# Kernel tuning notes

Hardware: AMD Instinct MI355X
Metric: run time of the kernel (lower is better)

## Reference

```python
import jax, jax.numpy as jnp
import numpy as np

N = 8192
D = 256  # out_feature; input feature dim must equal this per forward math
NEG_BIG = -9e15


def setup_inputs() -> dict:
    key = jax.random.key(0)
    k1, k2, k3 = jax.random.split(key, 3)
    inp = jax.random.normal(k1, (N, D), dtype=jnp.float32)
    adj = jax.random.randint(k2, (N, N), 0, 2, dtype=jnp.int32)
    # attention parameter A: [2*D, 1], xavier-uniform-like scale
    limit = np.sqrt(6.0 / (2 * D + 1)) * np.sqrt(2.0)  # gain('relu') = sqrt(2)
    A = jax.random.uniform(k3, (2 * D, 1), dtype=jnp.float32, minval=-limit, maxval=limit)
    return {"input": inp, "adj": adj, "A": A}


def reference(input, adj, A):
    d = input.shape[-1]
    h1 = input @ A[d:, :]   # [N, 1]
    h2 = input @ A[:d, :]   # [N, 1]
    e = h1 + h2.T           # [N, N] broadcast add
    att = jnp.where(adj > 0, e, jnp.asarray(NEG_BIG, e.dtype))
    att = jax.nn.softmax(att, axis=-1)
    return att @ input      # [N, D]
```

## Files before the change

kernel.cpp:

```cpp
#include <hip/hip_runtime.h>
#include <hip/hip_bf16.h>
#include <stdint.h>

typedef __attribute__((ext_vector_type(8))) short bf16x8;
typedef __attribute__((ext_vector_type(4))) float f32x4;

#define NN 8192
#define DF 256
#define BM 32
#define BK 64
#define KSPLIT 2
#define KCH (NN / KSPLIT)
#define NT (KCH / BK)

static __device__ __forceinline__ unsigned short f2bf(float f) {
  union { float f; unsigned u; } v; v.f = f;
  unsigned r = (v.u + 0x7FFFu + ((v.u >> 16) & 1u)) >> 16;
  return (unsigned short)r;
}

static __device__ __forceinline__ void gl_lds16(const void* g, void* l) {
  __builtin_amdgcn_global_load_lds(
      (const __attribute__((address_space(1))) void*)g,
      (__attribute__((address_space(3))) void*)l, 16, 0, 0);
}

__global__ void k_h2(const float* __restrict__ input, const float* __restrict__ A,
                     float* __restrict__ h2) {
  int gw = (blockIdx.x * blockDim.x + threadIdx.x) >> 6;
  int lane = threadIdx.x & 63;
  float4 x = *reinterpret_cast<const float4*>(&input[(size_t)gw * DF + lane * 4]);
  float4 a = *reinterpret_cast<const float4*>(&A[lane * 4]);
  float p = x.x * a.x + x.y * a.y + x.z * a.z + x.w * a.w;
#pragma unroll
  for (int off = 32; off > 0; off >>= 1) p += __shfl_down(p, off, 64);
  if (lane == 0) h2[gw] = p;
}

__global__ void k_max(const float* __restrict__ h2, float* __restrict__ Mout) {
  __shared__ float sm[4];
  float m = -3.0e38f;
  for (int i = threadIdx.x; i < NN; i += 256) m = fmaxf(m, h2[i]);
#pragma unroll
  for (int off = 32; off > 0; off >>= 1) m = fmaxf(m, __shfl_down(m, off, 64));
  int lane = threadIdx.x & 63, wid = threadIdx.x >> 6;
  if (lane == 0) sm[wid] = m;
  __syncthreads();
  if (threadIdx.x == 0)
    Mout[0] = fmaxf(fmaxf(sm[0], sm[1]), fmaxf(sm[2], sm[3]));
}

__global__ void k_s(const float* __restrict__ h2, const float* __restrict__ Mp,
                    float* __restrict__ sF, unsigned short* __restrict__ sT) {
  int j = blockIdx.x * 256 + threadIdx.x;
  float s = expf(h2[j] - Mp[0]);
  sF[j] = s;
  sT[j] = f2bf(s);
}

__global__ void k_xst(const float* __restrict__ input, const float* __restrict__ sF,
                      unsigned short* __restrict__ XsT) {
  int b = blockIdx.x;
  int jb = b >> 2, cb = b & 3;
  int t = threadIdx.x;
  int j0 = jb * 64 + (t & 15) * 4;
  int c0 = cb * 64 + (t >> 4) * 4;
  float4 x[4]; float s[4];
#pragma unroll
  for (int ii = 0; ii < 4; ii++) {
    x[ii] = *reinterpret_cast<const float4*>(&input[(size_t)(j0 + ii) * DF + c0]);
    s[ii] = sF[j0 + ii];
  }
#pragma unroll
  for (int q = 0; q < 4; q++) {
    ushort4 o;
    o.x = f2bf(reinterpret_cast<const float*>(&x[0])[q] * s[0]);
    o.y = f2bf(reinterpret_cast<const float*>(&x[1])[q] * s[1]);
    o.z = f2bf(reinterpret_cast<const float*>(&x[2])[q] * s[2]);
    o.w = f2bf(reinterpret_cast<const float*>(&x[3])[q] * s[3]);
    *reinterpret_cast<ushort4*>(&XsT[(size_t)(c0 + q) * NN + j0]) = o;
  }
}

__global__ __launch_bounds__(512, 2) void k_gemm(
    const int* __restrict__ adj, const unsigned short* __restrict__ XsT,
    const unsigned short* __restrict__ sT, float* __restrict__ C0,
    float* __restrict__ C1, float* __restrict__ denomPart) {
  __shared__ __align__(16) char Al[3][BM * BK * 4];

  const int tid = threadIdx.x;
  const int lane = tid & 63;
  const int wid = tid >> 6;
  const int wrow = wid >> 2;
  const int wcol = wid & 3;
  const int l15 = lane & 15;
  const int l4 = lane >> 4;

  const int bx = blockIdx.x;
  const int swz = (bx & 7) * 64 + (bx >> 3);
  const int kidx = swz >> 8;
  const int rb = swz & 255;
  const int kbeg = kidx * KCH;
  float* __restrict__ Cout = kidx ? C1 : C0;

  const int srow = tid >> 4;
  const int skb = ((tid & 15) * 16) ^ ((srow & 7) << 4);
  const int* sA = adj + (int64_t)(rb * BM + srow) * NN + kbeg + (skb >> 2);
  char* dstw = (char*)&Al[0][0] + wid * 1024;

  const unsigned short* Bb[4];
#pragma unroll
  for (int n = 0; n < 4; n++) {
    int c = wcol * 64 + n * 16 + l15;
    Bb[n] = XsT + (int64_t)c * NN + kbeg + l4 * 8;
  }
  const unsigned short* Sb = sT + kbeg + l4 * 8;

  const int arow_l = wrow * 16 + l15;
  const int aoff = (arow_l * 256 + l4 * 32) ^ ((arow_l & 7) << 4);

  bf16x8 regB[8];
  bf16x8 sv0, sv1;
  f32x4 acc[4] = {{0,0,0,0},{0,0,0,0},{0,0,0,0},{0,0,0,0}};
  f32x4 accD = {0, 0, 0, 0};

  auto stage = [&](int t, int buf) {
    gl_lds16(sA + t * BK, dstw + buf * 8192);
  };
  auto loadB = [&](int t) {
#pragma unroll
    for (int n = 0; n < 4; n++) {
      regB[n * 2 + 0] = *reinterpret_cast<const bf16x8*>(Bb[n] + t * BK);
      regB[n * 2 + 1] = *reinterpret_cast<const bf16x8*>(Bb[n] + t * BK + 32);
    }
    sv0 = *reinterpret_cast<const bf16x8*>(Sb + t * BK);
    sv1 = *reinterpret_cast<const bf16x8*>(Sb + t * BK + 32);
  };

  stage(0, 0);
  stage(1, 1);
  loadB(0);
  asm volatile("s_waitcnt vmcnt(0)" ::: "memory");
  __builtin_amdgcn_s_barrier();

  int bufc = 0, bufs = 2;
  for (int t = 0; t < NT; ++t) {
    const int t2 = (t + 2 < NT) ? t + 2 : NT - 1;
    const int t1 = (t + 1 < NT) ? t + 1 : NT - 1;
    stage(t2, bufs);

    const char* ab = (const char*)&Al[0][0] + bufc * 8192;
    int4 a0 = *reinterpret_cast<const int4*>(ab + (aoff));
    int4 a1 = *reinterpret_cast<const int4*>(ab + (aoff ^ 16));
    int4 a2 = *reinterpret_cast<const int4*>(ab + (aoff + 128));
    int4 a3 = *reinterpret_cast<const int4*>(ab + ((aoff + 128) ^ 16));
#pragma unroll
    for (int kk = 0; kk < 2; kk++) {
      union { unsigned u[4]; bf16x8 v; } A;
      const int4 lo = kk ? a2 : a0;
      const int4 hi = kk ? a3 : a1;
      A.u[0] = (unsigned)(lo.x + (lo.y << 16)) * 0x3F80u;
      A.u[1] = (unsigned)(lo.z + (lo.w << 16)) * 0x3F80u;
      A.u[2] = (unsigned)(hi.x + (hi.y << 16)) * 0x3F80u;
      A.u[3] = (unsigned)(hi.z + (hi.w << 16)) * 0x3F80u;
      if (wcol == 0) {
        accD = __builtin_amdgcn_mfma_f32_16x16x32_bf16(A.v, kk ? sv1 : sv0,
                                                       accD, 0, 0, 0);
      }
#pragma unroll
      for (int n = 0; n < 4; n++)
        acc[n] = __builtin_amdgcn_mfma_f32_16x16x32_bf16(A.v, regB[n * 2 + kk],
                                                         acc[n], 0, 0, 0);
    }

    loadB(t1);
    asm volatile("s_waitcnt vmcnt(11)" ::: "memory");
    __builtin_amdgcn_s_barrier();

    bufc = (bufc == 2) ? 0 : bufc + 1;
    bufs = (bufs == 2) ? 0 : bufs + 1;
  }

  const int row0 = rb * BM + wrow * 16 + l4 * 4;
#pragma unroll
  for (int n = 0; n < 4; n++) {
    int col = wcol * 64 + n * 16 + l15;
#pragma unroll
    for (int q = 0; q < 4; q++)
      Cout[(size_t)(row0 + q) * DF + col] = acc[n][q];
  }
  if (wcol == 0 && l15 == 0) {
#pragma unroll
    for (int q = 0; q < 4; q++)
      denomPart[kidx * NN + row0 + q] = accD[q];
  }
}

__global__ void k_norm(float* __restrict__ out, const float* __restrict__ C1,
                       const float* __restrict__ denomPart) {
  int e4 = blockIdx.x * 256 + threadIdx.x;
  size_t base = (size_t)e4 * 4;
  int row = (int)(base >> 8);
  float4 a = *reinterpret_cast<const float4*>(&out[base]);
  float4 b = *reinterpret_cast<const float4*>(&C1[base]);
  float inv = 1.0f / (denomPart[row] + denomPart[NN + row]);
  float4 r;
  r.x = (a.x + b.x) * inv;
  r.y = (a.y + b.y) * inv;
  r.z = (a.z + b.z) * inv;
  r.w = (a.w + b.w) * inv;
  *reinterpret_cast<float4*>(&out[base]) = r;
}

extern "C" void kernel_launch(void* const* d_in, const int* in_sizes, int n_in,
                              void* d_out, int out_size, void* d_ws, size_t ws_size,
                              hipStream_t stream) {
  const float* input = (const float*)d_in[0];
  const int* adj = (const int*)d_in[1];
  const float* A = (const float*)d_in[2];
  float* out = (float*)d_out;

  char* ws = (char*)d_ws;
  float* h2 = (float*)(ws + 0);
  float* Mv = (float*)(ws + 32768);
  float* sF = (float*)(ws + 33024);
  unsigned short* sT = (unsigned short*)(ws + 65792);
  unsigned short* XsT = (unsigned short*)(ws + 82176);
  float* C1 = (float*)(ws + 82176 + 4194304);
  float* denomPart = (float*)(ws + 82176 + 4194304 + 8388608);

  k_h2<<<dim3(NN / 4), dim3(256), 0, stream>>>(input, A, h2);
  k_max<<<dim3(1), dim3(256), 0, stream>>>(h2, Mv);
  k_s<<<dim3(NN / 256), dim3(256), 0, stream>>>(h2, Mv, sF, sT);
  k_xst<<<dim3((NN / 64) * (DF / 64)), dim3(256), 0, stream>>>(input, sF, XsT);
  k_gemm<<<dim3((NN / BM) * KSPLIT), dim3(512), 0, stream>>>(adj, XsT, sT, out, C1,
                                                             denomPart);
  k_norm<<<dim3(NN * DF / 1024), dim3(256), 0, stream>>>(out, C1, denomPart);
}
```

Baseline: 552.4 us.

## Stage XsT tiles into LDS with pre-tiled swizzled layout, 4-wave blocks, BK=32

The GEMM now loads the scaled-input B operand into LDS via global_load_lds from a pre-tiled, swizzled XsT layout written by k_xst, instead of each wave loading B fragments straight into registers. Blocks shrink to 4 waves, each computing both 16-row M tiles against 64 columns, which doubles B reuse per LDS read. BK drops to 32 to fit the larger per-stage LDS footprint, and the s vector is staged once into LDS. Separately, the max reduction is merged into k_s, removing one launch at the cost of every block redoing the full max scan.

```diff
diff --git a/kernel.cpp b/kernel.cpp
--- a/kernel.cpp
+++ b/kernel.cpp
@@ -8,10 +8,16 @@
 #define NN 8192
 #define DF 256
 #define BM 32
-#define BK 64
+#define BK 32
 #define KSPLIT 2
 #define KCH (NN / KSPLIT)
 #define NT (KCH / BK)
+#define NTILES_G (NN / BK)
+#define TILEA 4096
+#define TILEB 16384
+#define TILE_LDS (TILEA + TILEB)
+#define STLDS_OFF (3 * TILE_LDS)
+#define LDS_TOTAL (STLDS_OFF + 8192)
 
 static __device__ __forceinline__ unsigned short f2bf(float f) {
   union { float f; unsigned u; } v; v.f = f;
@@ -37,7 +43,8 @@
   if (lane == 0) h2[gw] = p;
 }
 
-__global__ void k_max(const float* __restrict__ h2, float* __restrict__ Mout) {
+__global__ void k_s(const float* __restrict__ h2, float* __restrict__ sF,
+                    unsigned short* __restrict__ sT) {
   __shared__ float sm[4];
   float m = -3.0e38f;
   for (int i = threadIdx.x; i < NN; i += 256) m = fmaxf(m, h2[i]);
@@ -46,20 +53,15 @@
   int lane = threadIdx.x & 63, wid = threadIdx.x >> 6;
   if (lane == 0) sm[wid] = m;
   __syncthreads();
-  if (threadIdx.x == 0)
-    Mout[0] = fmaxf(fmaxf(sm[0], sm[1]), fmaxf(sm[2], sm[3]));
-}
-
-__global__ void k_s(const float* __restrict__ h2, const float* __restrict__ Mp,
-                    float* __restrict__ sF, unsigned short* __restrict__ sT) {
+  float M = fmaxf(fmaxf(sm[0], sm[1]), fmaxf(sm[2], sm[3]));
   int j = blockIdx.x * 256 + threadIdx.x;
-  float s = expf(h2[j] - Mp[0]);
+  float s = expf(h2[j] - M);
   sF[j] = s;
   sT[j] = f2bf(s);
 }
 
 __global__ void k_xst(const float* __restrict__ input, const float* __restrict__ sF,
-                      unsigned short* __restrict__ XsT) {
+                      char* __restrict__ XsTb) {
   int b = blockIdx.x;
   int jb = b >> 2, cb = b & 3;
   int t = threadIdx.x;
@@ -73,26 +75,27 @@
   }
 #pragma unroll
   for (int q = 0; q < 4; q++) {
+    int c = c0 + q;
     ushort4 o;
     o.x = f2bf(reinterpret_cast<const float*>(&x[0])[q] * s[0]);
     o.y = f2bf(reinterpret_cast<const float*>(&x[1])[q] * s[1]);
     o.z = f2bf(reinterpret_cast<const float*>(&x[2])[q] * s[2]);
     o.w = f2bf(reinterpret_cast<const float*>(&x[3])[q] * s[3]);
-    *reinterpret_cast<ushort4*>(&XsT[(size_t)(c0 + q) * NN + j0]) = o;
-  }
-}
-
-__global__ __launch_bounds__(512, 2) void k_gemm(
-    const int* __restrict__ adj, const unsigned short* __restrict__ XsT,
+    size_t addr = (size_t)(j0 >> 5) * TILEB + (c & 127) * 128 + (c >> 7) * 64 +
+                  (((j0 & 31) * 2) ^ ((c & 3) << 4));
+    *reinterpret_cast<ushort4*>(XsTb + addr) = o;
+  }
+}
+
+__global__ __launch_bounds__(256, 2) void k_gemm(
+    const int* __restrict__ adj, const char* __restrict__ XsTb,
     const unsigned short* __restrict__ sT, float* __restrict__ C0,
     float* __restrict__ C1, float* __restrict__ denomPart) {
-  __shared__ __align__(16) char Al[3][BM * BK * 4];
+  __shared__ __align__(16) char lds[LDS_TOTAL];
 
   const int tid = threadIdx.x;
   const int lane = tid & 63;
   const int wid = tid >> 6;
-  const int wrow = wid >> 2;
-  const int wcol = wid & 3;
   const int l15 = lane & 15;
   const int l4 = lane >> 4;
 
@@ -101,98 +104,105 @@
   const int kidx = swz >> 8;
   const int rb = swz & 255;
   const int kbeg = kidx * KCH;
+  const int kt0 = kidx * NT;
   float* __restrict__ Cout = kidx ? C1 : C0;
 
-  const int srow = tid >> 4;
-  const int skb = ((tid & 15) * 16) ^ ((srow & 7) << 4);
-  const int* sA = adj + (int64_t)(rb * BM + srow) * NN + kbeg + (skb >> 2);
-  char* dstw = (char*)&Al[0][0] + wid * 1024;
-
-  const unsigned short* Bb[4];
+  const int srow = tid >> 3;
+  const int sbyte = ((tid & 7) * 16) ^ ((srow & 7) << 4);
+  const char* pA = (const char*)adj +
+                   ((size_t)(rb * BM + srow) * NN + kbeg) * 4 + sbyte;
+  const char* pB = XsTb + (size_t)kt0 * TILEB + tid * 16;
+  const char* pS = (const char*)sT + (size_t)kbeg * 2 + tid * 16;
+  char* dstT = lds + tid * 16;
+
+  const int arow0 = l15;
+  int aoff[2];
+#pragma unroll
+  for (int m = 0; m < 2; m++) {
+    int row = m * 16 + arow0;
+    aoff[m] = row * 128 + ((l4 * 32) ^ ((row & 7) << 4));
+  }
+  int boff[4];
 #pragma unroll
   for (int n = 0; n < 4; n++) {
-    int c = wcol * 64 + n * 16 + l15;
-    Bb[n] = XsT + (int64_t)c * NN + kbeg + l4 * 8;
-  }
-  const unsigned short* Sb = sT + kbeg + l4 * 8;
-
-  const int arow_l = wrow * 16 + l15;
-  const int aoff = (arow_l * 256 + l4 * 32) ^ ((arow_l & 7) << 4);
-
-  bf16x8 regB[8];
-  bf16x8 sv0, sv1;
-  f32x4 acc[4] = {{0,0,0,0},{0,0,0,0},{0,0,0,0},{0,0,0,0}};
-  f32x4 accD = {0, 0, 0, 0};
-
-  auto stage = [&](int t, int buf) {
-    gl_lds16(sA + t * BK, dstw + buf * 8192);
+    int c = wid * 64 + n * 16 + l15;
+    boff[n] = (c & 127) * 128 + ((c >> 7) << 6) + ((l4 * 16) ^ ((c & 3) << 4));
+  }
+  const char* sTl = lds + STLDS_OFF + l4 * 16;
+
+  f32x4 acc[2][4] = {{{0,0,0,0},{0,0,0,0},{0,0,0,0},{0,0,0,0}},
+                     {{0,0,0,0},{0,0,0,0},{0,0,0,0},{0,0,0,0}}};
+  f32x4 accD[2] = {{0,0,0,0},{0,0,0,0}};
+
+  auto stage = [&](int tk, int buf) {
+    char* d = dstT + buf * TILE_LDS;
+    gl_lds16(pA + (size_t)tk * 128, d);
+#pragma unroll
+    for (int o = 0; o < 4; o++)
+      gl_lds16(pB + (size_t)tk * TILEB + o * 4096, d + TILEA + o * 4096);
   };
-  auto loadB = [&](int t) {
-#pragma unroll
-    for (int n = 0; n < 4; n++) {
-      regB[n * 2 + 0] = *reinterpret_cast<const bf16x8*>(Bb[n] + t * BK);
-      regB[n * 2 + 1] = *reinterpret_cast<const bf16x8*>(Bb[n] + t * BK + 32);
-    }
-    sv0 = *reinterpret_cast<const bf16x8*>(Sb + t * BK);
-    sv1 = *reinterpret_cast<const bf16x8*>(Sb + t * BK + 32);
-  };
-
+
+  gl_lds16(pS, lds + STLDS_OFF + tid * 16);
+  gl_lds16(pS + 4096, lds + STLDS_OFF + 4096 + tid * 16);
   stage(0, 0);
   stage(1, 1);
-  loadB(0);
-  asm volatile("s_waitcnt vmcnt(0)" ::: "memory");
+  asm volatile("s_waitcnt vmcnt(5)" ::: "memory");
   __builtin_amdgcn_s_barrier();
 
-  int bufc = 0, bufs = 2;
+  int bcur = 0, bnx2 = 2;
   for (int t = 0; t < NT; ++t) {
-    const int t2 = (t + 2 < NT) ? t + 2 : NT - 1;
-    const int t1 = (t + 1 < NT) ? t + 1 : NT - 1;
-    stage(t2, bufs);
-
-    const char* ab = (const char*)&Al[0][0] + bufc * 8192;
-    int4 a0 = *reinterpret_cast<const int4*>(ab + (aoff));
-    int4 a1 = *reinterpret_cast<const int4*>(ab + (aoff ^ 16));
-    int4 a2 = *reinterpret_cast<const int4*>(ab + (aoff + 128));
-    int4 a3 = *reinterpret_cast<const int4*>(ab + ((aoff + 128) ^ 16));
-#pragma unroll
-    for (int kk = 0; kk < 2; kk++) {
+    const int tk2 = (t + 2 < NT) ? t + 2 : NT - 1;
+    stage(tk2, bnx2);
+
+    const char* ab = lds + bcur * TILE_LDS;
+    const char* bb = ab + TILEA;
+    bf16x8 Am[2];
+#pragma unroll
+    for (int m = 0; m < 2; m++) {
+      int4 lo = *reinterpret_cast<const int4*>(ab + aoff[m]);
+      int4 hi = *reinterpret_cast<const int4*>(ab + (aoff[m] ^ 16));
       union { unsigned u[4]; bf16x8 v; } A;
-      const int4 lo = kk ? a2 : a0;
-      const int4 hi = kk ? a3 : a1;
       A.u[0] = (unsigned)(lo.x + (lo.y << 16)) * 0x3F80u;
       A.u[1] = (unsigned)(lo.z + (lo.w << 16)) * 0x3F80u;
       A.u[2] = (unsigned)(hi.x + (hi.y << 16)) * 0x3F80u;
       A.u[3] = (unsigned)(hi.z + (hi.w << 16)) * 0x3F80u;
-      if (wcol == 0) {
-        accD = __builtin_amdgcn_mfma_f32_16x16x32_bf16(A.v, kk ? sv1 : sv0,
-                                                       accD, 0, 0, 0);
-      }
-#pragma unroll
-      for (int n = 0; n < 4; n++)
-        acc[n] = __builtin_amdgcn_mfma_f32_16x16x32_bf16(A.v, regB[n * 2 + kk],
-                                                         acc[n], 0, 0, 0);
-    }
-
-    loadB(t1);
-    asm volatile("s_waitcnt vmcnt(11)" ::: "memory");
+      Am[m] = A.v;
+    }
+    bf16x8 sv = *reinterpret_cast<const bf16x8*>(sTl + t * 64);
+#pragma unroll
+    for (int n = 0; n < 4; n++) {
+      bf16x8 Bf = *reinterpret_cast<const bf16x8*>(bb + boff[n]);
+#pragma unroll
+      for (int m = 0; m < 2; m++)
+        acc[m][n] = __builtin_amdgcn_mfma_f32_16x16x32_bf16(Am[m], Bf,
+                                                            acc[m][n], 0, 0, 0);
+    }
+#pragma unroll
+    for (int m = 0; m < 2; m++)
+      accD[m] = __builtin_amdgcn_mfma_f32_16x16x32_bf16(Am[m], sv,
+                                                        accD[m], 0, 0, 0);
+
+    asm volatile("s_waitcnt vmcnt(5)" ::: "memory");
     __builtin_amdgcn_s_barrier();
-
-    bufc = (bufc == 2) ? 0 : bufc + 1;
-    bufs = (bufs == 2) ? 0 : bufs + 1;
-  }
-
-  const int row0 = rb * BM + wrow * 16 + l4 * 4;
-#pragma unroll
-  for (int n = 0; n < 4; n++) {
-    int col = wcol * 64 + n * 16 + l15;
-#pragma unroll
-    for (int q = 0; q < 4; q++)
-      Cout[(size_t)(row0 + q) * DF + col] = acc[n][q];
-  }
-  if (wcol == 0 && l15 == 0) {
-#pragma unroll
-    for (int q = 0; q < 4; q++)
-      denomPart[kidx * NN + row0 + q] = accD[q];
+    bcur = (bcur == 2) ? 0 : bcur + 1;
+    bnx2 = (bnx2 == 2) ? 0 : bnx2 + 1;
+  }
+
+#pragma unroll
+  for (int m = 0; m < 2; m++) {
+    int row0 = rb * BM + m * 16 + l4 * 4;
+#pragma unroll
+    for (int n = 0; n < 4; n++) {
+      int col = wid * 64 + n * 16 + l15;
+#pragma unroll
+      for (int q = 0; q < 4; q++)
+        Cout[(size_t)(row0 + q) * DF + col] = acc[m][n][q];
+    }
+    if (wid == 0 && l15 == 0) {
+#pragma unroll
+      for (int q = 0; q < 4; q++)
+        denomPart[kidx * NN + row0 + q] = accD[m][q];
+    }
   }
 }
 
@@ -222,18 +232,16 @@
 
   char* ws = (char*)d_ws;
   float* h2 = (float*)(ws + 0);
-  float* Mv = (float*)(ws + 32768);
   float* sF = (float*)(ws + 33024);
   unsigned short* sT = (unsigned short*)(ws + 65792);
-  unsigned short* XsT = (unsigned short*)(ws + 82176);
+  char* XsTb = (char*)(ws + 82176);
   float* C1 = (float*)(ws + 82176 + 4194304);
   float* denomPart = (float*)(ws + 82176 + 4194304 + 8388608);
 
   k_h2<<<dim3(NN / 4), dim3(256), 0, stream>>>(input, A, h2);
-  k_max<<<dim3(1), dim3(256), 0, stream>>>(h2, Mv);
-  k_s<<<dim3(NN / 256), dim3(256), 0, stream>>>(h2, Mv, sF, sT);
-  k_xst<<<dim3((NN / 64) * (DF / 64)), dim3(256), 0, stream>>>(input, sF, XsT);
-  k_gemm<<<dim3((NN / BM) * KSPLIT), dim3(512), 0, stream>>>(adj, XsT, sT, out, C1,
+  k_s<<<dim3(NN / 256), dim3(256), 0, stream>>>(h2, sF, sT);
+  k_xst<<<dim3((NN / 64) * (DF / 64)), dim3(256), 0, stream>>>(input, sF, XsTb);
+  k_gemm<<<dim3((NN / BM) * KSPLIT), dim3(256), 0, stream>>>(adj, XsTb, sT, out, C1,
                                                              denomPart);
   k_norm<<<dim3(NN * DF / 1024), dim3(256), 0, stream>>>(out, C1, denomPart);
 }
```

Result: faster. 450.1 us (-18.5%).

## Replace LDS-staged adjacency GEMM with direct global loads and fuse max into exp kernel

Applied to the files above, without the earlier changes.

The GEMM kernel drops the triple-buffered LDS staging of the adjacency tile and the barriers. Each 256-thread block now handles 16 rows and loads adj, XsT and sT straight from global memory into registers, with a 2x unrolled loop. Separately, the global max of h2 is recomputed inside every k_s block, which removes the single-block max kernel launch. The adj stream is what dominates, and without software pipelining the kernel relies on occupancy and the compiler to hide load latency. Smaller 16-row tiles also mean XsT is re-read twice as often.

```diff
diff --git a/kernel.cpp b/kernel.cpp
--- a/kernel.cpp
+++ b/kernel.cpp
@@ -7,22 +7,14 @@
 
 #define NN 8192
 #define DF 256
-#define BM 32
-#define BK 64
 #define KSPLIT 2
 #define KCH (NN / KSPLIT)
-#define NT (KCH / BK)
+#define KSTEPS (KCH / 32)
 
 static __device__ __forceinline__ unsigned short f2bf(float f) {
   union { float f; unsigned u; } v; v.f = f;
   unsigned r = (v.u + 0x7FFFu + ((v.u >> 16) & 1u)) >> 16;
   return (unsigned short)r;
-}
-
-static __device__ __forceinline__ void gl_lds16(const void* g, void* l) {
-  __builtin_amdgcn_global_load_lds(
-      (const __attribute__((address_space(1))) void*)g,
-      (__attribute__((address_space(3))) void*)l, 16, 0, 0);
 }
 
 __global__ void k_h2(const float* __restrict__ input, const float* __restrict__ A,
@@ -37,7 +29,8 @@
   if (lane == 0) h2[gw] = p;
 }
 
-__global__ void k_max(const float* __restrict__ h2, float* __restrict__ Mout) {
+__global__ void k_s(const float* __restrict__ h2, float* __restrict__ sF,
+                    unsigned short* __restrict__ sT) {
   __shared__ float sm[4];
   float m = -3.0e38f;
   for (int i = threadIdx.x; i < NN; i += 256) m = fmaxf(m, h2[i]);
@@ -46,14 +39,9 @@
   int lane = threadIdx.x & 63, wid = threadIdx.x >> 6;
   if (lane == 0) sm[wid] = m;
   __syncthreads();
-  if (threadIdx.x == 0)
-    Mout[0] = fmaxf(fmaxf(sm[0], sm[1]), fmaxf(sm[2], sm[3]));
-}
-
-__global__ void k_s(const float* __restrict__ h2, const float* __restrict__ Mp,
-                    float* __restrict__ sF, unsigned short* __restrict__ sT) {
+  float M = fmaxf(fmaxf(sm[0], sm[1]), fmaxf(sm[2], sm[3]));
   int j = blockIdx.x * 256 + threadIdx.x;
-  float s = expf(h2[j] - Mp[0]);
+  float s = expf(h2[j] - M);
   sF[j] = s;
   sT[j] = f2bf(s);
 }
@@ -82,114 +70,68 @@
   }
 }
 
-__global__ __launch_bounds__(512, 2) void k_gemm(
+__global__ __launch_bounds__(256, 4) void k_gemm(
     const int* __restrict__ adj, const unsigned short* __restrict__ XsT,
     const unsigned short* __restrict__ sT, float* __restrict__ C0,
     float* __restrict__ C1, float* __restrict__ denomPart) {
-  __shared__ __align__(16) char Al[3][BM * BK * 4];
-
   const int tid = threadIdx.x;
   const int lane = tid & 63;
   const int wid = tid >> 6;
-  const int wrow = wid >> 2;
-  const int wcol = wid & 3;
   const int l15 = lane & 15;
   const int l4 = lane >> 4;
 
   const int bx = blockIdx.x;
-  const int swz = (bx & 7) * 64 + (bx >> 3);
-  const int kidx = swz >> 8;
-  const int rb = swz & 255;
+  const int kidx = bx & 1;
+  const int rg = bx >> 1;
+  const int r0 = rg * 16;
   const int kbeg = kidx * KCH;
   float* __restrict__ Cout = kidx ? C1 : C0;
 
-  const int srow = tid >> 4;
-  const int skb = ((tid & 15) * 16) ^ ((srow & 7) << 4);
-  const int* sA = adj + (int64_t)(rb * BM + srow) * NN + kbeg + (skb >> 2);
-  char* dstw = (char*)&Al[0][0] + wid * 1024;
+  const int* pA = adj + (size_t)(r0 + l15) * NN + kbeg + l4 * 8;
+  const unsigned short* pB0 = XsT + (size_t)(wid * 64 + 0 * 16 + l15) * NN + kbeg + l4 * 8;
+  const unsigned short* pB1 = XsT + (size_t)(wid * 64 + 1 * 16 + l15) * NN + kbeg + l4 * 8;
+  const unsigned short* pB2 = XsT + (size_t)(wid * 64 + 2 * 16 + l15) * NN + kbeg + l4 * 8;
+  const unsigned short* pB3 = XsT + (size_t)(wid * 64 + 3 * 16 + l15) * NN + kbeg + l4 * 8;
+  const unsigned short* pS = sT + kbeg + l4 * 8;
 
-  const unsigned short* Bb[4];
-#pragma unroll
-  for (int n = 0; n < 4; n++) {
-    int c = wcol * 64 + n * 16 + l15;
-    Bb[n] = XsT + (int64_t)c * NN + kbeg + l4 * 8;
-  }
-  const unsigned short* Sb = sT + kbeg + l4 * 8;
+  f32x4 acc0 = {0,0,0,0}, acc1 = {0,0,0,0}, acc2 = {0,0,0,0}, acc3 = {0,0,0,0};
+  f32x4 accD = {0,0,0,0};
 
-  const int arow_l = wrow * 16 + l15;
-  const int aoff = (arow_l * 256 + l4 * 32) ^ ((arow_l & 7) << 4);
-
-  bf16x8 regB[8];
-  bf16x8 sv0, sv1;
-  f32x4 acc[4] = {{0,0,0,0},{0,0,0,0},{0,0,0,0},{0,0,0,0}};
-  f32x4 accD = {0, 0, 0, 0};
-
-  auto stage = [&](int t, int buf) {
-    gl_lds16(sA + t * BK, dstw + buf * 8192);
-  };
-  auto loadB = [&](int t) {
-#pragma unroll
-    for (int n = 0; n < 4; n++) {
-      regB[n * 2 + 0] = *reinterpret_cast<const bf16x8*>(Bb[n] + t * BK);
-      regB[n * 2 + 1] = *reinterpret_cast<const bf16x8*>(Bb[n] + t * BK + 32);
+#pragma unroll 2
+  for (int t = 0; t < KSTEPS; ++t) {
+    const int ko = t * 32;
+    int4 lo = *reinterpret_cast<const int4*>(pA + ko);
+    int4 hi = *reinterpret_cast<const int4*>(pA + ko + 4);
+    bf16x8 b0 = *reinterpret_cast<const bf16x8*>(pB0 + ko);
+    bf16x8 b1 = *reinterpret_cast<const bf16x8*>(pB1 + ko);
+    bf16x8 b2 = *reinterpret_cast<const bf16x8*>(pB2 + ko);
+    bf16x8 b3 = *reinterpret_cast<const bf16x8*>(pB3 + ko);
+    union { unsigned u[4]; bf16x8 v; } A;
+    A.u[0] = (unsigned)(lo.x + (lo.y << 16)) * 0x3F80u;
+    A.u[1] = (unsigned)(lo.z + (lo.w << 16)) * 0x3F80u;
+    A.u[2] = (unsigned)(hi.x + (hi.y << 16)) * 0x3F80u;
+    A.u[3] = (unsigned)(hi.z + (hi.w << 16)) * 0x3F80u;
+    acc0 = __builtin_amdgcn_mfma_f32_16x16x32_bf16(A.v, b0, acc0, 0, 0, 0);
+    acc1 = __builtin_amdgcn_mfma_f32_16x16x32_bf16(A.v, b1, acc1, 0, 0, 0);
+    acc2 = __builtin_amdgcn_mfma_f32_16x16x32_bf16(A.v, b2, acc2, 0, 0, 0);
+    acc3 = __builtin_amdgcn_mfma_f32_16x16x32_bf16(A.v, b3, acc3, 0, 0, 0);
+    if (wid == 0) {
+      bf16x8 sv = *reinterpret_cast<const bf16x8*>(pS + ko);
+      accD = __builtin_amdgcn_mfma_f32_16x16x32_bf16(A.v, sv, accD, 0, 0, 0);
     }
-    sv0 = *reinterpret_cast<const bf16x8*>(Sb + t * BK);
-    sv1 = *reinterpret_cast<const bf16x8*>(Sb + t * BK + 32);
-  };
-
-  stage(0, 0);
-  stage(1, 1);
-  loadB(0);
-  asm volatile("s_waitcnt vmcnt(0)" ::: "memory");
-  __builtin_amdgcn_s_barrier();
-
-  int bufc = 0, bufs = 2;
-  for (int t = 0; t < NT; ++t) {
-    const int t2 = (t + 2 < NT) ? t + 2 : NT - 1;
-    const int t1 = (t + 1 < NT) ? t + 1 : NT - 1;
-    stage(t2, bufs);
-
-    const char* ab = (const char*)&Al[0][0] + bufc * 8192;
-    int4 a0 = *reinterpret_cast<const int4*>(ab + (aoff));
-    int4 a1 = *reinterpret_cast<const int4*>(ab + (aoff ^ 16));
-    int4 a2 = *reinterpret_cast<const int4*>(ab + (aoff + 128));
-    int4 a3 = *reinterpret_cast<const int4*>(ab + ((aoff + 128) ^ 16));
-#pragma unroll
-    for (int kk = 0; kk < 2; kk++) {
-      union { unsigned u[4]; bf16x8 v; } A;
-      const int4 lo = kk ? a2 : a0;
-      const int4 hi = kk ? a3 : a1;
-      A.u[0] = (unsigned)(lo.x + (lo.y << 16)) * 0x3F80u;
-      A.u[1] = (unsigned)(lo.z + (lo.w << 16)) * 0x3F80u;
-      A.u[2] = (unsigned)(hi.x + (hi.y << 16)) * 0x3F80u;
-      A.u[3] = (unsigned)(hi.z + (hi.w << 16)) * 0x3F80u;
-      if (wcol == 0) {
-        accD = __builtin_amdgcn_mfma_f32_16x16x32_bf16(A.v, kk ? sv1 : sv0,
-                                                       accD, 0, 0, 0);
-      }
-#pragma unroll
-      for (int n = 0; n < 4; n++)
-        acc[n] = __builtin_amdgcn_mfma_f32_16x16x32_bf16(A.v, regB[n * 2 + kk],
-                                                         acc[n], 0, 0, 0);
-    }
-
-    loadB(t1);
-    asm volatile("s_waitcnt vmcnt(11)" ::: "memory");
-    __builtin_amdgcn_s_barrier();
-
-    bufc = (bufc == 2) ? 0 : bufc + 1;
-    bufs = (bufs == 2) ? 0 : bufs + 1;
   }
 
-  const int row0 = rb * BM + wrow * 16 + l4 * 4;
+  const int row0 = r0 + l4 * 4;
+  const int col0 = wid * 64 + l15;
 #pragma unroll
-  for (int n = 0; n < 4; n++) {
-    int col = wcol * 64 + n * 16 + l15;
-#pragma unroll
-    for (int q = 0; q < 4; q++)
-      Cout[(size_t)(row0 + q) * DF + col] = acc[n][q];
+  for (int q = 0; q < 4; q++) {
+    float* cr = Cout + (size_t)(row0 + q) * DF + col0;
+    cr[0]  = acc0[q];
+    cr[16] = acc1[q];
+    cr[32] = acc2[q];
+    cr[48] = acc3[q];
   }
-  if (wcol == 0 && l15 == 0) {
+  if (wid == 0 && l15 == 0) {
 #pragma unroll
     for (int q = 0; q < 4; q++)
       denomPart[kidx * NN + row0 + q] = accD[q];
@@ -222,7 +164,6 @@
 
   char* ws = (char*)d_ws;
   float* h2 = (float*)(ws + 0);
-  float* Mv = (float*)(ws + 32768);
   float* sF = (float*)(ws + 33024);
   unsigned short* sT = (unsigned short*)(ws + 65792);
   unsigned short* XsT = (unsigned short*)(ws + 82176);
@@ -230,10 +171,9 @@
   float* denomPart = (float*)(ws + 82176 + 4194304 + 8388608);
 
   k_h2<<<dim3(NN / 4), dim3(256), 0, stream>>>(input, A, h2);
-  k_max<<<dim3(1), dim3(256), 0, stream>>>(h2, Mv);
-  k_s<<<dim3(NN / 256), dim3(256), 0, stream>>>(h2, Mv, sF, sT);
+  k_s<<<dim3(NN / 256), dim3(256), 0, stream>>>(h2, sF, sT);
   k_xst<<<dim3((NN / 64) * (DF / 64)), dim3(256), 0, stream>>>(input, sF, XsT);
-  k_gemm<<<dim3((NN / BM) * KSPLIT), dim3(512), 0, stream>>>(adj, XsT, sT, out, C1,
+  k_gemm<<<dim3((NN / 16) * KSPLIT), dim3(256), 0, stream>>>(adj, XsT, sT, out, C1,
                                                              denomPart);
   k_norm<<<dim3(NN * DF / 1024), dim3(256), 0, stream>>>(out, C1, denomPart);
 }
```

New measurement: 686.9 us. +24.4%, slower.
